# Kernel optimization log

Hardware: AMD Instinct MI355X
Metric: run time of the kernel (lower is better)

The kernel has to match this reference:

```python
import jax, jax.numpy as jnp
import numpy as np

# dims: Q queries, K hops (topk), N relation groups, M padded nodes/group
Q, K, N, M = 64, 2, 32, 64
E, D, R, S = 256, 1024, 200, 8192  # embs_size, model_size, n_rel, seq positions


def setup_inputs() -> dict:
    key = jax.random.key(0)
    ks = jax.random.split(key, 10)
    hidden_states = jax.random.normal(ks[0], (S, D), jnp.float32)
    nodes = jax.random.normal(ks[1], (Q, K, N, M, E), jnp.float32)
    # ragged groups: zero-pad beyond a random valid length (mirrors F.pad + stack)
    lengths = jax.random.randint(ks[2], (Q, K, N), 1, M + 1)
    valid = jnp.arange(M)[None, None, None, :] < lengths[..., None]
    nodes = nodes * valid[..., None]
    prob_idx = jax.random.randint(ks[3], (Q, K, N), 0, R)
    gnn_idx = jnp.arange(Q, dtype=jnp.int32)          # gnn_mask positions
    rel_idx = jnp.arange(Q, dtype=jnp.int32) + Q      # rel_mask positions (disjoint)
    sc = lambda fan: float(1.0 / np.sqrt(fan))
    u = lambda k, shp, fan: jax.random.uniform(k, shp, jnp.float32, -sc(fan), sc(fan))
    Wc = u(ks[4], (D, R), D); bc = jnp.zeros((R,), jnp.float32)
    Wq = u(ks[5], (D, D), D); bq = jnp.zeros((D,), jnp.float32)
    Wn = u(ks[6], (E, D), E); bn = jnp.zeros((D,), jnp.float32)
    Wg = u(ks[7], (E, D), E); bg = jnp.zeros((D,), jnp.float32)
    return {"hidden_states": hidden_states, "nodes": nodes, "prob_idx": prob_idx,
            "gnn_idx": gnn_idx, "rel_idx": rel_idx,
            "Wc": Wc, "bc": bc, "Wq": Wq, "bq": bq,
            "Wn": Wn, "bn": bn, "Wg": Wg, "bg": bg}


def reference(hidden_states, nodes, prob_idx, gnn_idx, rel_idx,
              Wc, bc, Wq, bq, Wn, bn, Wg, bg):
    Qn, Kn, Nn, Mn, En = nodes.shape
    # classification_head: Linear + Softmax over relations
    rel_prob = jax.nn.softmax(hidden_states[rel_idx] @ Wc + bc, axis=1)  # [Q,R]
    # gather per-group relation probabilities (extract_values_from_tensor)
    probs = jnp.take_along_axis(rel_prob, prob_idx.reshape(Qn, Kn * Nn), axis=1)
    probs = probs.reshape(Qn, Kn, Nn)                                     # [Q,K,N]
    # mask from first feature of padded node embeddings (as in calculate_scores)
    mask = nodes[..., 0] != 0                                             # [Q,K,N,M]
    # query_reprj and nodes_reprj (Linear + Tanh)
    gq = jnp.tanh(hidden_states[gnn_idx] @ Wq + bq)                       # [Q,D]
    gn = jnp.tanh(jnp.einsum('qknme,ed->qknmd', nodes, Wn) + bn)          # [Q,K,N,M,D]
    dots = jnp.einsum('qknmd,qd->qknm', gn, gq)                           # [Q,K,N,M]
    attn = jax.nn.softmax(dots, axis=3)            # softmax over nodes within group
    logits = attn * probs[..., None] / 0.1         # scale by group prob / temperature
    # global softmax over all (group, node) slots per (query, hop)
    wa = jax.nn.softmax(logits.reshape(Qn, Kn, Nn * Mn), axis=-1)
    wa = wa.reshape(Qn, Kn, Nn, Mn)
    wa = jnp.where(mask, wa, 0.0)
    # weighted mean over the flattened N*M slots, then mean over topk hops
    mean_emb = jnp.mean(nodes * wa[..., None], axis=(2, 3))               # [Q,K,E]
    pooled = mean_emb.mean(axis=1)                                        # [Q,E]
    out = jnp.tanh(pooled @ Wg + bg)                                      # gnn_reprj
    return hidden_states.at[gnn_idx].add(out)
```

## Files before the change

### kernel.cpp

```cpp
#include <hip/hip_runtime.h>
#include <hip/hip_bf16.h>
#include <math.h>

#define QDIM 64
#define KDIM 2
#define NDIM 32
#define MDIM 64
#define EDIM 256
#define DDIM 1024
#define RDIM 200
#define SDIM 8192
#define GCOUNT (QDIM * KDIM * NDIM)

typedef short short8_t __attribute__((ext_vector_type(8)));
typedef float f32x4 __attribute__((ext_vector_type(4)));

__device__ __forceinline__ float tanh_c(float x) {
    float e = __expf(2.0f * x);
    return 1.0f - 2.0f * __builtin_amdgcn_rcpf(1.0f + e);
}

__device__ __forceinline__ uint32_t f2bf(float f) {
    uint32_t u = __float_as_uint(f);
    return (u + 0x7fffu + ((u >> 16) & 1u)) >> 16;
}
__device__ __forceinline__ float bf2f(unsigned short h) {
    return __uint_as_float(((uint32_t)h) << 16);
}

__global__ __launch_bounds__(256) void prologue_kernel(
    const float* __restrict__ hs, float* __restrict__ out,
    const float* __restrict__ Wn, short* __restrict__ wnpk,
    const int* __restrict__ gnn_idx, const float* __restrict__ Wq,
    const float* __restrict__ bq, float* __restrict__ gqo,
    const int* __restrict__ rel_idx, const float* __restrict__ Wc,
    const float* __restrict__ bc, float* __restrict__ rel_prob,
    const float* __restrict__ nodes, int* __restrict__ nvarr) {
    const int b = blockIdx.x, t = threadIdx.x;
    __shared__ float row[DDIM];
    __shared__ float arr[256];

    if (b < 2048) {
        const float4* src = (const float4*)hs;
        float4* dst = (float4*)out;
        int i = b * 256 + t;
#pragma unroll
        for (int r = 0; r < 4; ++r) dst[i + r * 524288] = src[i + r * 524288];
    } else if (b < 2176) {
        int tid = (b - 2048) * 256 + t;
        int lane = tid & 63, ks = (tid >> 6) & 7, ntg = tid >> 9;
        int low = lane & 15, hi = lane >> 4;
        short8_t o;
#pragma unroll
        for (int j = 0; j < 8; ++j) {
            int k = ks * 32 + hi * 8 + j;
            int d = ntg * 16 + low;
            o[j] = (short)f2bf(Wn[(size_t)k * DDIM + d]);
        }
        *(short8_t*)(wnpk + (size_t)tid * 8) = o;
    } else if (b < 2432) {
        int bb = b - 2176;
        int q = bb >> 2, seg = bb & 3;
        const float* src = hs + (size_t)gnn_idx[q] * DDIM;
        for (int i = t; i < DDIM; i += 256) row[i] = src[i];
        __syncthreads();
        int d = seg * 256 + t;
        float a = bq[d];
#pragma unroll 8
        for (int k = 0; k < DDIM; ++k) a += row[k] * Wq[(size_t)k * DDIM + d];
        gqo[(size_t)q * DDIM + d] = tanh_c(a);
    } else if (b < 2496) {
        int q = b - 2432;
        const float* src = hs + (size_t)rel_idx[q] * DDIM;
        for (int i = t; i < DDIM; i += 256) row[i] = src[i];
        __syncthreads();
        float lg = -INFINITY;
        if (t < RDIM) {
            float a = bc[t];
            for (int k = 0; k < DDIM; ++k) a += row[k] * Wc[(size_t)k * RDIM + t];
            lg = a;
        }
        arr[t] = lg;
        __syncthreads();
        for (int s = 128; s > 0; s >>= 1) {
            if (t < s) arr[t] = fmaxf(arr[t], arr[t + s]);
            __syncthreads();
        }
        float mx = arr[0];
        __syncthreads();
        float ex = (t < RDIM) ? __expf(lg - mx) : 0.0f;
        arr[t] = ex;
        __syncthreads();
        for (int s = 128; s > 0; s >>= 1) {
            if (t < s) arr[t] += arr[t + s];
            __syncthreads();
        }
        float sm = arr[0];
        if (t < RDIM) rel_prob[q * RDIM + t] = ex / sm;
    } else {
        int g = (b - 2496) * 4 + (t >> 6);
        int lane = t & 63;
        float f0 = nodes[(size_t)g * (MDIM * EDIM) + (size_t)lane * EDIM];
        unsigned long long mk = __ballot(f0 != 0.0f);
        if (lane == 0) nvarr[g] = __popcll(mk);
    }
}

__global__ __launch_bounds__(64) void pack_jobs(const int* __restrict__ nvarr,
                                                const float* __restrict__ bn,
                                                const float* __restrict__ gq,
                                                int4* __restrict__ glist4,
                                                float* __restrict__ cqarr) {
    int q = blockIdx.x, t = threadIdx.x;
    __shared__ int lists[4][64];
    __shared__ int cnt[4];
    float cp = 0.f;
#pragma unroll
    for (int i = 0; i < 16; ++i) {
        int d = i * 64 + t;
        cp += tanh_c(bn[d]) * gq[(size_t)q * DDIM + d];
    }
#pragma unroll
    for (int off = 32; off > 0; off >>= 1) cp += __shfl_xor(cp, off);
    if (t == 0) cqarr[q] = cp;

    if (t < 4) cnt[t] = 0;
    __syncthreads();
    int g = q * 64 + t;
    int nv = nvarr[g];
    int mt = (nv + 15) >> 4;
    if (mt < 1) mt = 1;
    if (mt > 4) mt = 4;
    int pos = atomicAdd(&cnt[mt - 1], 1);
    lists[mt - 1][pos] = g;
    __syncthreads();
    if (t == 0) {
        int c1 = cnt[0], c2 = cnt[1], c3 = cnt[2], c4 = cnt[3];
        int i1 = 0, i2 = 0, i3 = 0, i4 = 0, j = 0;
        int4* outp = glist4 + q * 64;
        const int D = GCOUNT;
        while (i4 < c4) outp[j++] = make_int4(lists[3][i4++] | (0 << 20), D, D, D);
        while (i3 < c3) {
            int g1 = (i1 < c1) ? lists[0][i1++] : D;
            outp[j++] = make_int4(lists[2][i3++] | (1 << 20), g1, D, D);
        }
        while (i2 + 1 < c2) {
            int a = lists[1][i2++], b2 = lists[1][i2++];
            outp[j++] = make_int4(a | (2 << 20), b2, D, D);
        }
        if (i2 < c2) {
            int a = lists[1][i2++];
            int b2 = (i1 < c1) ? lists[0][i1++] : D;
            int c = (i1 < c1) ? lists[0][i1++] : D;
            outp[j++] = make_int4(a | (3 << 20), b2, c, D);
        }
        while (i1 < c1) {
            int a = lists[0][i1++];
            int b2 = (i1 < c1) ? lists[0][i1++] : D;
            int c = (i1 < c1) ? lists[0][i1++] : D;
            int d2 = (i1 < c1) ? lists[0][i1++] : D;
            outp[j++] = make_int4(a | (4 << 20), b2, c, d2);
        }
        while (j < 64) outp[j++] = make_int4(-1, -1, -1, -1);
    }
}

template <int U0, int NU>
__device__ __forceinline__ void epi(int g, int q, float (&dacc)[4][4],
                                    short8_t (&af)[4][8], float cq, float* scr,
                                    const float* __restrict__ rel_prob,
                                    const int* __restrict__ prob_idx,
                                    float* __restrict__ gvec, float* __restrict__ gden,
                                    float* __restrict__ gmx, int lane) {
    const int low = lane & 15, hi = lane >> 4;
    constexpr int TAIL = 64 - NU * 16;
    float mx = -INFINITY;
#pragma unroll
    for (int u = U0; u < U0 + NU; ++u)
#pragma unroll
        for (int jj = 0; jj < 4; ++jj) mx = fmaxf(mx, dacc[u][jj]);
    mx = fmaxf(mx, __shfl_xor(mx, 16));
    mx = fmaxf(mx, __shfl_xor(mx, 32));
    if (TAIL > 0) mx = fmaxf(mx, cq);
    float exv[4][4];
    float sm = 0.f;
#pragma unroll
    for (int u = U0; u < U0 + NU; ++u)
#pragma unroll
        for (int jj = 0; jj < 4; ++jj) {
            exv[u][jj] = __expf(dacc[u][jj] - mx);
            sm += exv[u][jj];
        }
    sm += __shfl_xor(sm, 16);
    sm += __shfl_xor(sm, 32);
    float ext = __expf(cq - mx);
    if (TAIL > 0) sm += (float)TAIL * ext;
    float pr = rel_prob[(size_t)q * RDIM + prob_idx[g >= GCOUNT ? 0 : g]];
    float p10 = pr * 10.0f / sm;
#pragma unroll
    for (int u = U0; u < U0 + NU; ++u)
#pragma unroll
        for (int jj = 0; jj < 4; ++jj) exv[u][jj] *= p10;
    float lgvt = ext * p10;
    float gm = -INFINITY;
#pragma unroll
    for (int u = U0; u < U0 + NU; ++u)
#pragma unroll
        for (int jj = 0; jj < 4; ++jj) gm = fmaxf(gm, exv[u][jj]);
    gm = fmaxf(gm, __shfl_xor(gm, 16));
    gm = fmaxf(gm, __shfl_xor(gm, 32));
    if (TAIL > 0) gm = fmaxf(gm, lgvt);
    float elv[4][4];
    float den = 0.f;
#pragma unroll
    for (int u = U0; u < U0 + NU; ++u)
#pragma unroll
        for (int jj = 0; jj < 4; ++jj) {
            elv[u][jj] = __expf(exv[u][jj] - gm);
            den += elv[u][jj];
        }
    den += __shfl_xor(den, 16);
    den += __shfl_xor(den, 32);
    if (TAIL > 0) den += (float)TAIL * __expf(lgvt - gm);
    if (lane == 0) {
        gden[g] = den;
        gmx[g] = gm;
    }
    float* lvarr = scr;
    float* mkarr = scr + 64;
    float* vb = scr + 128;
    if (low == 0) {
#pragma unroll
        for (int u = U0; u < U0 + NU; ++u)
#pragma unroll
            for (int jj = 0; jj < 4; ++jj) lvarr[u * 16 + hi * 4 + jj] = elv[u][jj];
    }
    asm volatile("s_waitcnt lgkmcnt(0)" ::: "memory");
    float lvm[4];
#pragma unroll
    for (int u = U0; u < U0 + NU; ++u) lvm[u] = lvarr[u * 16 + low] * mkarr[u * 16 + low];
#pragma unroll
    for (int ks = 0; ks < 8; ++ks) {
        float acj[8];
#pragma unroll
        for (int j = 0; j < 8; ++j) acj[j] = 0.f;
#pragma unroll
        for (int u = U0; u < U0 + NU; ++u) {
#pragma unroll
            for (int j = 0; j < 8; ++j)
                acj[j] += bf2f((unsigned short)af[u][ks][j]) * lvm[u];
        }
#pragma unroll
        for (int j = 0; j < 8; ++j) {
            float a = acj[j];
            a += __shfl_xor(a, 1);
            a += __shfl_xor(a, 2);
            a += __shfl_xor(a, 4);
            a += __shfl_xor(a, 8);
            if (low == 0) vb[ks * 32 + hi * 8 + j] = a;
        }
    }
    asm volatile("s_waitcnt lgkmcnt(0)" ::: "memory");
    float4 ov = ((const float4*)vb)[lane];
    *(float4*)(gvec + (size_t)g * EDIM + lane * 4) = ov;
    asm volatile("s_waitcnt lgkmcnt(0)" ::: "memory");
}

#define STEP(CUR, NXT, NTG)                                                              \
    {                                                                                    \
        int pn_ = (NTG) + 1;                                                             \
        pn_ = pn_ > 63 ? 63 : pn_;                                                       \
        const short8_t* pp_ = bbase + (size_t)pn_ * 512;                                 \
        _Pragma("unroll") for (int ks = 0; ks < 8; ++ks) NXT[ks] = pp_[ks * 64];         \
        float2 pv_ = pairs[(NTG) * 16 + low];                                            \
        f32x4 a0 = {0.f, 0.f, 0.f, 0.f}, a1 = a0, a2 = a0, a3 = a0;                      \
        _Pragma("unroll") for (int ks = 0; ks < 8; ++ks) {                               \
            a0 = __builtin_amdgcn_mfma_f32_16x16x32_bf16(af[0][ks], CUR[ks], a0, 0, 0, 0); \
            a1 = __builtin_amdgcn_mfma_f32_16x16x32_bf16(af[1][ks], CUR[ks], a1, 0, 0, 0); \
            a2 = __builtin_amdgcn_mfma_f32_16x16x32_bf16(af[2][ks], CUR[ks], a2, 0, 0, 0); \
            a3 = __builtin_amdgcn_mfma_f32_16x16x32_bf16(af[3][ks], CUR[ks], a3, 0, 0, 0); \
        }                                                                                \
        float bnv_ = pv_.x, gqv_ = pv_.y;                                                \
        _Pragma("unroll") for (int jj = 0; jj < 4; ++jj) {                               \
            dacc[0][jj] += tanh_c(a0[jj] + bnv_) * gqv_;                                 \
            dacc[1][jj] += tanh_c(a1[jj] + bnv_) * gqv_;                                 \
            dacc[2][jj] += tanh_c(a2[jj] + bnv_) * gqv_;                                 \
            dacc[3][jj] += tanh_c(a3[jj] + bnv_) * gqv_;                                 \
        }                                                                                \
    }

__global__ __launch_bounds__(64, 2) void phase1_mfma(
    const float* __restrict__ nodes, const short* __restrict__ wnpk,
    const float* __restrict__ bn, const float* __restrict__ gq,
    const float* __restrict__ rel_prob, const int* __restrict__ prob_idx,
    const int4* __restrict__ glist4, const float* __restrict__ cqarr,
    float* __restrict__ gvec, float* __restrict__ gden, float* __restrict__ gmx) {
    __shared__ alignas(16) char transit[8192];
    __shared__ float scr[384];
    int4 jb = glist4[blockIdx.x];
    if (jb.x < 0) return;
    const int shape = (jb.x >> 20) & 7;
    const int g0 = jb.x & 0xFFFF, g1 = jb.y, g2 = jb.z, g3 = jb.w;
    const int q = g0 >> 6;
    const int lane = threadIdx.x & 63;
    const int low = lane & 15, hi = lane >> 4;
    const float cqv = cqarr[q];

    const unsigned tabs[5] = {0x30201000u, 0x01201000u, 0x11011000u, 0x02011000u,
                              0x03020100u};
    const unsigned tb = tabs[shape];

    short8_t af[4][8];
#pragma unroll
    for (int u = 0; u < 4; ++u) {
        int byte_ = (tb >> (u * 8)) & 0xFF;
        int slot = byte_ & 0xF, tile = byte_ >> 4;
        int gs = slot == 0 ? g0 : slot == 1 ? g1 : slot == 2 ? g2 : g3;
        int lg = (gs >= GCOUNT) ? 0 : gs;
        const float4* src = (const float4*)(nodes + ((size_t)lg * MDIM + tile * 16) * EDIM);
#pragma unroll
        for (int i = 0; i < 16; ++i) {
            int idx4 = i * 64 + lane;
            float4 v = src[idx4];
            int r = idx4 >> 6, c4 = idx4 & 63;
            int off = (r * 512 + c4 * 8) ^ ((r & 7) << 4);
            uint32_t w0 = f2bf(v.x) | (f2bf(v.y) << 16);
            uint32_t w1 = f2bf(v.z) | (f2bf(v.w) << 16);
            *(uint2*)(transit + off) = make_uint2(w0, w1);
        }
        asm volatile("s_waitcnt lgkmcnt(0)" ::: "memory");
#pragma unroll
        for (int ks = 0; ks < 8; ++ks) {
            int off = (low * 512 + ks * 64 + hi * 16) ^ ((low & 7) << 4);
            af[u][ks] = *(const short8_t*)(transit + off);
        }
        asm volatile("s_waitcnt lgkmcnt(0)" ::: "memory");
    }

    {
        const float* gqrow = gq + (size_t)q * DDIM;
        float2* pw = (float2*)transit;
#pragma unroll
        for (int i = 0; i < 16; ++i) {
            int d = i * 64 + lane;
            float2 v;
            v.x = bn[d];
            v.y = gqrow[d];
            pw[d] = v;
        }
        asm volatile("s_waitcnt lgkmcnt(0)" ::: "memory");
    }
    const float2* pairs = (const float2*)transit;

    float dacc[4][4];
#pragma unroll
    for (int u = 0; u < 4; ++u)
#pragma unroll
        for (int jj = 0; jj < 4; ++jj) dacc[u][jj] = 0.f;
    const short8_t* bbase = (const short8_t*)wnpk + lane;
    short8_t bA[8], bB[8];
#pragma unroll
    for (int ks = 0; ks < 8; ++ks) bA[ks] = bbase[ks * 64];
    for (int it = 0; it < 32; ++it) {
        STEP(bA, bB, 2 * it);
        STEP(bB, bA, 2 * it + 1);
    }

#pragma unroll
    for (int u = 0; u < 4; ++u)
#pragma unroll
        for (int jj = 0; jj < 4; ++jj) {
            float v = dacc[u][jj];
            v += __shfl_xor(v, 1);
            v += __shfl_xor(v, 2);
            v += __shfl_xor(v, 4);
            v += __shfl_xor(v, 8);
            dacc[u][jj] = v;
        }

    if (hi == 0) {
#pragma unroll
        for (int u = 0; u < 4; ++u) {
            unsigned short s0 = (unsigned short)af[u][0][0];
            (scr + 64)[u * 16 + low] = ((s0 & 0x7fffu) != 0) ? 1.0f : 0.0f;
        }
    }
    asm volatile("s_waitcnt lgkmcnt(0)" ::: "memory");

    switch (shape) {
        case 0:
            epi<0, 4>(g0, q, dacc, af, cqv, scr, rel_prob, prob_idx, gvec, gden, gmx, lane);
            break;
        case 1:
            epi<0, 3>(g0, q, dacc, af, cqv, scr, rel_prob, prob_idx, gvec, gden, gmx, lane);
            epi<3, 1>(g1, q, dacc, af, cqv, scr, rel_prob, prob_idx, gvec, gden, gmx, lane);
            break;
        case 2:
            epi<0, 2>(g0, q, dacc, af, cqv, scr, rel_prob, prob_idx, gvec, gden, gmx, lane);
            epi<2, 2>(g1, q, dacc, af, cqv, scr, rel_prob, prob_idx, gvec, gden, gmx, lane);
            break;
        case 3:
            epi<0, 2>(g0, q, dacc, af, cqv, scr, rel_prob, prob_idx, gvec, gden, gmx, lane);
            epi<2, 1>(g1, q, dacc, af, cqv, scr, rel_prob, prob_idx, gvec, gden, gmx, lane);
            epi<3, 1>(g2, q, dacc, af, cqv, scr, rel_prob, prob_idx, gvec, gden, gmx, lane);
            break;
        default:
            epi<0, 1>(g0, q, dacc, af, cqv, scr, rel_prob, prob_idx, gvec, gden, gmx, lane);
            epi<1, 1>(g1, q, dacc, af, cqv, scr, rel_prob, prob_idx, gvec, gden, gmx, lane);
            epi<2, 1>(g2, q, dacc, af, cqv, scr, rel_prob, prob_idx, gvec, gden, gmx, lane);
            epi<3, 1>(g3, q, dacc, af, cqv, scr, rel_prob, prob_idx, gvec, gden, gmx, lane);
            break;
    }
}

__global__ __launch_bounds__(256) void combine_kernel(const float* __restrict__ gvec,
                                                      const float* __restrict__ gden,
                                                      const float* __restrict__ gmx,
                                                      float* __restrict__ memb) {
    int qk = blockIdx.x, t = threadIdx.x;
    __shared__ float sgm[NDIM], sden[NDIM];
    if (t < NDIM) {
        sgm[t] = gmx[qk * NDIM + t];
        sden[t] = gden[qk * NDIM + t];
    }
    __syncthreads();
    float gm = -INFINITY;
    for (int n = 0; n < NDIM; ++n) gm = fmaxf(gm, sgm[n]);
    float gs = 0.f;
    for (int n = 0; n < NDIM; ++n) gs += sden[n] * __expf(sgm[n] - gm);
    float me = 0.f;
    for (int n = 0; n < NDIM; ++n)
        me += gvec[(size_t)(qk * NDIM + n) * EDIM + t] * __expf(sgm[n] - gm);
    memb[(size_t)qk * EDIM + t] = me / (gs * (float)(NDIM * MDIM));
}

__global__ __launch_bounds__(256) void out_kernel(const float* __restrict__ memb,
                                                  const float* __restrict__ Wg,
                                                  const float* __restrict__ bg,
                                                  const int* __restrict__ gnn_idx,
                                                  float* __restrict__ out) {
    int q = blockIdx.x, t = threadIdx.x;
    __shared__ float pooled[EDIM];
    pooled[t] = 0.5f * (memb[(size_t)(q * 2 + 0) * EDIM + t] + memb[(size_t)(q * 2 + 1) * EDIM + t]);
    __syncthreads();
    float4 a = ((const float4*)bg)[t];
    const float4* Wg4 = (const float4*)Wg;
    for (int e = 0; e < EDIM; ++e) {
        float p = pooled[e];
        float4 w = Wg4[(size_t)e * (DDIM / 4) + t];
        a.x += p * w.x; a.y += p * w.y; a.z += p * w.z; a.w += p * w.w;
    }
    float4* op = (float4*)(out + (size_t)gnn_idx[q] * DDIM);
    float4 cur = op[t];
    cur.x += tanh_c(a.x);
    cur.y += tanh_c(a.y);
    cur.z += tanh_c(a.z);
    cur.w += tanh_c(a.w);
    op[t] = cur;
}

extern "C" void kernel_launch(void* const* d_in, const int* in_sizes, int n_in,
                              void* d_out, int out_size, void* d_ws, size_t ws_size,
                              hipStream_t stream) {
    const float* hs = (const float*)d_in[0];
    const float* nodes = (const float*)d_in[1];
    const int* prob_idx = (const int*)d_in[2];
    const int* gnn_idx = (const int*)d_in[3];
    const int* rel_idx = (const int*)d_in[4];
    const float* Wc = (const float*)d_in[5];
    const float* bc = (const float*)d_in[6];
    const float* Wq = (const float*)d_in[7];
    const float* bq = (const float*)d_in[8];
    const float* Wn = (const float*)d_in[9];
    const float* bn = (const float*)d_in[10];
    const float* Wg = (const float*)d_in[11];
    const float* bg = (const float*)d_in[12];
    float* out = (float*)d_out;
    float* ws = (float*)d_ws;

    float* relprob = ws;
    float* gqbuf = ws + 16384;
    float* gvec = gqbuf + 65536;
    float* gdenA = gvec + 1048832;
    float* gmaxA = gdenA + 4352;
    float* membuf = gmaxA + 4352;
    short* wnpk = (short*)(membuf + 32768);
    int* nvarr = (int*)(ws + 1303296);
    int4* glist4 = (int4*)(ws + 1307392);
    float* cqarr = ws + 1323776;

    prologue_kernel<<<3520, 256, 0, stream>>>(hs, out, Wn, wnpk, gnn_idx, Wq, bq,
                                              gqbuf, rel_idx, Wc, bc, relprob,
                                              nodes, nvarr);
    pack_jobs<<<QDIM, 64, 0, stream>>>(nvarr, bn, gqbuf, glist4, cqarr);
    phase1_mfma<<<GCOUNT, 64, 0, stream>>>(nodes, wnpk, bn, gqbuf, relprob,
                                           prob_idx, glist4, cqarr, gvec, gdenA, gmaxA);
    combine_kernel<<<QDIM * KDIM, 256, 0, stream>>>(gvec, gdenA, gmaxA, membuf);
    out_kernel<<<QDIM, 256, 0, stream>>>(membuf, Wg, bg, gnn_idx, out);
}
```

Before: 301.0 us.

## Split each MFMA job across two waves and pack two jobs per block

The phase1 kernel moves from one 64-thread wave per job, each holding four 16-row node tiles, to 256-thread blocks that process two jobs. Each wave now holds two tiles, which halves the per-wave A-fragment registers and MFMA chain length and exposes more parallel waves. The group softmax epilogue and weighted-sum reduction are rebuilt to go through shared memory with block barriers, and bias/query pairs are loaded once per block. In exchange, each wave re-reads the full Wn stream for only two tiles, so total Wn traffic per job doubles. The change also adds barriers and LDS usage that may limit occupancy.

```diff
diff --git a/kernel.cpp b/kernel.cpp
--- a/kernel.cpp
+++ b/kernel.cpp
@@ -165,251 +165,234 @@
     }
 }
 
-template <int U0, int NU>
-__device__ __forceinline__ void epi(int g, int q, float (&dacc)[4][4],
-                                    short8_t (&af)[4][8], float cq, float* scr,
-                                    const float* __restrict__ rel_prob,
-                                    const int* __restrict__ prob_idx,
-                                    float* __restrict__ gvec, float* __restrict__ gden,
-                                    float* __restrict__ gmx, int lane) {
-    const int low = lane & 15, hi = lane >> 4;
-    constexpr int TAIL = 64 - NU * 16;
-    float mx = -INFINITY;
-#pragma unroll
-    for (int u = U0; u < U0 + NU; ++u)
-#pragma unroll
-        for (int jj = 0; jj < 4; ++jj) mx = fmaxf(mx, dacc[u][jj]);
-    mx = fmaxf(mx, __shfl_xor(mx, 16));
-    mx = fmaxf(mx, __shfl_xor(mx, 32));
-    if (TAIL > 0) mx = fmaxf(mx, cq);
-    float exv[4][4];
-    float sm = 0.f;
-#pragma unroll
-    for (int u = U0; u < U0 + NU; ++u)
-#pragma unroll
-        for (int jj = 0; jj < 4; ++jj) {
-            exv[u][jj] = __expf(dacc[u][jj] - mx);
-            sm += exv[u][jj];
-        }
-    sm += __shfl_xor(sm, 16);
-    sm += __shfl_xor(sm, 32);
-    float ext = __expf(cq - mx);
-    if (TAIL > 0) sm += (float)TAIL * ext;
-    float pr = rel_prob[(size_t)q * RDIM + prob_idx[g >= GCOUNT ? 0 : g]];
-    float p10 = pr * 10.0f / sm;
-#pragma unroll
-    for (int u = U0; u < U0 + NU; ++u)
-#pragma unroll
-        for (int jj = 0; jj < 4; ++jj) exv[u][jj] *= p10;
-    float lgvt = ext * p10;
-    float gm = -INFINITY;
-#pragma unroll
-    for (int u = U0; u < U0 + NU; ++u)
-#pragma unroll
-        for (int jj = 0; jj < 4; ++jj) gm = fmaxf(gm, exv[u][jj]);
-    gm = fmaxf(gm, __shfl_xor(gm, 16));
-    gm = fmaxf(gm, __shfl_xor(gm, 32));
-    if (TAIL > 0) gm = fmaxf(gm, lgvt);
-    float elv[4][4];
-    float den = 0.f;
-#pragma unroll
-    for (int u = U0; u < U0 + NU; ++u)
-#pragma unroll
-        for (int jj = 0; jj < 4; ++jj) {
-            elv[u][jj] = __expf(exv[u][jj] - gm);
-            den += elv[u][jj];
-        }
-    den += __shfl_xor(den, 16);
-    den += __shfl_xor(den, 32);
-    if (TAIL > 0) den += (float)TAIL * __expf(lgvt - gm);
-    if (lane == 0) {
-        gden[g] = den;
-        gmx[g] = gm;
-    }
-    float* lvarr = scr;
-    float* mkarr = scr + 64;
-    float* vb = scr + 128;
-    if (low == 0) {
-#pragma unroll
-        for (int u = U0; u < U0 + NU; ++u)
-#pragma unroll
-            for (int jj = 0; jj < 4; ++jj) lvarr[u * 16 + hi * 4 + jj] = elv[u][jj];
-    }
-    asm volatile("s_waitcnt lgkmcnt(0)" ::: "memory");
-    float lvm[4];
-#pragma unroll
-    for (int u = U0; u < U0 + NU; ++u) lvm[u] = lvarr[u * 16 + low] * mkarr[u * 16 + low];
-#pragma unroll
-    for (int ks = 0; ks < 8; ++ks) {
-        float acj[8];
-#pragma unroll
-        for (int j = 0; j < 8; ++j) acj[j] = 0.f;
-#pragma unroll
-        for (int u = U0; u < U0 + NU; ++u) {
-#pragma unroll
-            for (int j = 0; j < 8; ++j)
-                acj[j] += bf2f((unsigned short)af[u][ks][j]) * lvm[u];
-        }
-#pragma unroll
-        for (int j = 0; j < 8; ++j) {
-            float a = acj[j];
-            a += __shfl_xor(a, 1);
-            a += __shfl_xor(a, 2);
-            a += __shfl_xor(a, 4);
-            a += __shfl_xor(a, 8);
-            if (low == 0) vb[ks * 32 + hi * 8 + j] = a;
-        }
-    }
-    asm volatile("s_waitcnt lgkmcnt(0)" ::: "memory");
-    float4 ov = ((const float4*)vb)[lane];
-    *(float4*)(gvec + (size_t)g * EDIM + lane * 4) = ov;
-    asm volatile("s_waitcnt lgkmcnt(0)" ::: "memory");
-}
-
-#define STEP(CUR, NXT, NTG)                                                              \
-    {                                                                                    \
-        int pn_ = (NTG) + 1;                                                             \
-        pn_ = pn_ > 63 ? 63 : pn_;                                                       \
-        const short8_t* pp_ = bbase + (size_t)pn_ * 512;                                 \
-        _Pragma("unroll") for (int ks = 0; ks < 8; ++ks) NXT[ks] = pp_[ks * 64];         \
-        float2 pv_ = pairs[(NTG) * 16 + low];                                            \
-        f32x4 a0 = {0.f, 0.f, 0.f, 0.f}, a1 = a0, a2 = a0, a3 = a0;                      \
-        _Pragma("unroll") for (int ks = 0; ks < 8; ++ks) {                               \
+#define STEP2(CUR, NXT, NTG)                                                               \
+    {                                                                                      \
+        int pn_ = (NTG) + 1;                                                               \
+        pn_ = pn_ > 63 ? 63 : pn_;                                                         \
+        const short8_t* pp_ = bbase + (size_t)pn_ * 512;                                   \
+        _Pragma("unroll") for (int ks = 0; ks < 8; ++ks) NXT[ks] = pp_[ks * 64];           \
+        float2 pv_ = pairs[(NTG)*16 + low];                                                \
+        f32x4 a0 = {0.f, 0.f, 0.f, 0.f}, a1 = a0;                                          \
+        _Pragma("unroll") for (int ks = 0; ks < 8; ++ks) {                                 \
             a0 = __builtin_amdgcn_mfma_f32_16x16x32_bf16(af[0][ks], CUR[ks], a0, 0, 0, 0); \
             a1 = __builtin_amdgcn_mfma_f32_16x16x32_bf16(af[1][ks], CUR[ks], a1, 0, 0, 0); \
-            a2 = __builtin_amdgcn_mfma_f32_16x16x32_bf16(af[2][ks], CUR[ks], a2, 0, 0, 0); \
-            a3 = __builtin_amdgcn_mfma_f32_16x16x32_bf16(af[3][ks], CUR[ks], a3, 0, 0, 0); \
-        }                                                                                \
-        float bnv_ = pv_.x, gqv_ = pv_.y;                                                \
-        _Pragma("unroll") for (int jj = 0; jj < 4; ++jj) {                               \
-            dacc[0][jj] += tanh_c(a0[jj] + bnv_) * gqv_;                                 \
-            dacc[1][jj] += tanh_c(a1[jj] + bnv_) * gqv_;                                 \
-            dacc[2][jj] += tanh_c(a2[jj] + bnv_) * gqv_;                                 \
-            dacc[3][jj] += tanh_c(a3[jj] + bnv_) * gqv_;                                 \
-        }                                                                                \
-    }
-
-__global__ __launch_bounds__(64, 2) void phase1_mfma(
+        }                                                                                  \
+        float bnv_ = pv_.x, gqv_ = pv_.y;                                                  \
+        _Pragma("unroll") for (int jj = 0; jj < 4; ++jj) {                                 \
+            dacc[0][jj] += tanh_c(a0[jj] + bnv_) * gqv_;                                   \
+            dacc[1][jj] += tanh_c(a1[jj] + bnv_) * gqv_;                                   \
+        }                                                                                  \
+    }
+
+__global__ __launch_bounds__(256, 3) void phase1_mfma(
     const float* __restrict__ nodes, const short* __restrict__ wnpk,
     const float* __restrict__ bn, const float* __restrict__ gq,
     const float* __restrict__ rel_prob, const int* __restrict__ prob_idx,
     const int4* __restrict__ glist4, const float* __restrict__ cqarr,
     float* __restrict__ gvec, float* __restrict__ gden, float* __restrict__ gmx) {
-    __shared__ alignas(16) char transit[8192];
-    __shared__ float scr[384];
-    int4 jb = glist4[blockIdx.x];
-    if (jb.x < 0) return;
-    const int shape = (jb.x >> 20) & 7;
-    const int g0 = jb.x & 0xFFFF, g1 = jb.y, g2 = jb.z, g3 = jb.w;
-    const int q = g0 >> 6;
-    const int lane = threadIdx.x & 63;
+    __shared__ alignas(16) char transit[4][8192];
+    __shared__ float2 pairs[DDIM];
+    __shared__ float vecu[8][EDIM];
+    __shared__ float dots_s[128];
+    __shared__ float lv_s[128];
+    __shared__ float mk_s[128];
+
+    const int tid = threadIdx.x;
+    const int w = tid >> 6, lane = tid & 63;
     const int low = lane & 15, hi = lane >> 4;
+
+    const int4 jb0 = glist4[2 * blockIdx.x];
+    const int4 jb1 = glist4[2 * blockIdx.x + 1];
+    if (jb0.x < 0 && jb1.x < 0) return;
+    const int4 jb = (w < 2) ? jb0 : jb1;
+    const bool live = jb.x >= 0;
+    const int q = ((jb0.x >= 0 ? jb0.x : jb1.x) & 0xFFFF) >> 6;
     const float cqv = cqarr[q];
 
     const unsigned tabs[5] = {0x30201000u, 0x01201000u, 0x11011000u, 0x02011000u,
                               0x03020100u};
-    const unsigned tb = tabs[shape];
-
-    short8_t af[4][8];
-#pragma unroll
-    for (int u = 0; u < 4; ++u) {
-        int byte_ = (tb >> (u * 8)) & 0xFF;
-        int slot = byte_ & 0xF, tile = byte_ >> 4;
-        int gs = slot == 0 ? g0 : slot == 1 ? g1 : slot == 2 ? g2 : g3;
-        int lg = (gs >= GCOUNT) ? 0 : gs;
-        const float4* src = (const float4*)(nodes + ((size_t)lg * MDIM + tile * 16) * EDIM);
-#pragma unroll
-        for (int i = 0; i < 16; ++i) {
-            int idx4 = i * 64 + lane;
-            float4 v = src[idx4];
-            int r = idx4 >> 6, c4 = idx4 & 63;
-            int off = (r * 512 + c4 * 8) ^ ((r & 7) << 4);
-            uint32_t w0 = f2bf(v.x) | (f2bf(v.y) << 16);
-            uint32_t w1 = f2bf(v.z) | (f2bf(v.w) << 16);
-            *(uint2*)(transit + off) = make_uint2(w0, w1);
-        }
-        asm volatile("s_waitcnt lgkmcnt(0)" ::: "memory");
-#pragma unroll
-        for (int ks = 0; ks < 8; ++ks) {
-            int off = (low * 512 + ks * 64 + hi * 16) ^ ((low & 7) << 4);
-            af[u][ks] = *(const short8_t*)(transit + off);
-        }
-        asm volatile("s_waitcnt lgkmcnt(0)" ::: "memory");
+    const int gA[4] = {jb.x & 0xFFFF, jb.y, jb.z, jb.w};
+    const unsigned tb = live ? tabs[(jb.x >> 20) & 7] : 0;
+
+    int usrc[2] = {GCOUNT, GCOUNT};
+    short8_t af[2][8];
+    if (live) {
+        char* ldsw = transit[w];
+#pragma unroll
+        for (int u2 = 0; u2 < 2; ++u2) {
+            int u = (w & 1) * 2 + u2;
+            int byte_ = (tb >> (u * 8)) & 0xFF;
+            int slot = byte_ & 0xF, tile = byte_ >> 4;
+            int gs = gA[slot];
+            usrc[u2] = gs;
+            int lg = (gs >= GCOUNT) ? 0 : gs;
+            const float4* src =
+                (const float4*)(nodes + ((size_t)lg * MDIM + tile * 16) * EDIM);
+#pragma unroll
+            for (int i = 0; i < 16; ++i) {
+                int idx4 = i * 64 + lane;
+                float4 v = src[idx4];
+                int r = idx4 >> 6, c4 = idx4 & 63;
+                int off = (r * 512 + c4 * 8) ^ ((r & 7) << 4);
+                uint32_t w0 = f2bf(v.x) | (f2bf(v.y) << 16);
+                uint32_t w1 = f2bf(v.z) | (f2bf(v.w) << 16);
+                *(uint2*)(ldsw + off) = make_uint2(w0, w1);
+            }
+            asm volatile("s_waitcnt lgkmcnt(0)" ::: "memory");
+#pragma unroll
+            for (int ks = 0; ks < 8; ++ks) {
+                int off = (low * 512 + ks * 64 + hi * 16) ^ ((low & 7) << 4);
+                af[u2][ks] = *(const short8_t*)(ldsw + off);
+            }
+            asm volatile("s_waitcnt lgkmcnt(0)" ::: "memory");
+        }
     }
 
     {
         const float* gqrow = gq + (size_t)q * DDIM;
-        float2* pw = (float2*)transit;
-#pragma unroll
-        for (int i = 0; i < 16; ++i) {
-            int d = i * 64 + lane;
-            float2 v;
-            v.x = bn[d];
-            v.y = gqrow[d];
-            pw[d] = v;
-        }
-        asm volatile("s_waitcnt lgkmcnt(0)" ::: "memory");
-    }
-    const float2* pairs = (const float2*)transit;
-
-    float dacc[4][4];
-#pragma unroll
-    for (int u = 0; u < 4; ++u)
-#pragma unroll
-        for (int jj = 0; jj < 4; ++jj) dacc[u][jj] = 0.f;
-    const short8_t* bbase = (const short8_t*)wnpk + lane;
-    short8_t bA[8], bB[8];
-#pragma unroll
-    for (int ks = 0; ks < 8; ++ks) bA[ks] = bbase[ks * 64];
-    for (int it = 0; it < 32; ++it) {
-        STEP(bA, bB, 2 * it);
-        STEP(bB, bA, 2 * it + 1);
-    }
-
-#pragma unroll
-    for (int u = 0; u < 4; ++u)
-#pragma unroll
-        for (int jj = 0; jj < 4; ++jj) {
-            float v = dacc[u][jj];
-            v += __shfl_xor(v, 1);
-            v += __shfl_xor(v, 2);
-            v += __shfl_xor(v, 4);
-            v += __shfl_xor(v, 8);
-            dacc[u][jj] = v;
-        }
-
-    if (hi == 0) {
-#pragma unroll
-        for (int u = 0; u < 4; ++u) {
-            unsigned short s0 = (unsigned short)af[u][0][0];
-            (scr + 64)[u * 16 + low] = ((s0 & 0x7fffu) != 0) ? 1.0f : 0.0f;
-        }
-    }
-    asm volatile("s_waitcnt lgkmcnt(0)" ::: "memory");
-
-    switch (shape) {
-        case 0:
-            epi<0, 4>(g0, q, dacc, af, cqv, scr, rel_prob, prob_idx, gvec, gden, gmx, lane);
-            break;
-        case 1:
-            epi<0, 3>(g0, q, dacc, af, cqv, scr, rel_prob, prob_idx, gvec, gden, gmx, lane);
-            epi<3, 1>(g1, q, dacc, af, cqv, scr, rel_prob, prob_idx, gvec, gden, gmx, lane);
-            break;
-        case 2:
-            epi<0, 2>(g0, q, dacc, af, cqv, scr, rel_prob, prob_idx, gvec, gden, gmx, lane);
-            epi<2, 2>(g1, q, dacc, af, cqv, scr, rel_prob, prob_idx, gvec, gden, gmx, lane);
-            break;
-        case 3:
-            epi<0, 2>(g0, q, dacc, af, cqv, scr, rel_prob, prob_idx, gvec, gden, gmx, lane);
-            epi<2, 1>(g1, q, dacc, af, cqv, scr, rel_prob, prob_idx, gvec, gden, gmx, lane);
-            epi<3, 1>(g2, q, dacc, af, cqv, scr, rel_prob, prob_idx, gvec, gden, gmx, lane);
-            break;
-        default:
-            epi<0, 1>(g0, q, dacc, af, cqv, scr, rel_prob, prob_idx, gvec, gden, gmx, lane);
-            epi<1, 1>(g1, q, dacc, af, cqv, scr, rel_prob, prob_idx, gvec, gden, gmx, lane);
-            epi<2, 1>(g2, q, dacc, af, cqv, scr, rel_prob, prob_idx, gvec, gden, gmx, lane);
-            epi<3, 1>(g3, q, dacc, af, cqv, scr, rel_prob, prob_idx, gvec, gden, gmx, lane);
-            break;
+#pragma unroll
+        for (int i = 0; i < 4; ++i) {
+            int d = tid + i * 256;
+            pairs[d] = make_float2(bn[d], gqrow[d]);
+        }
+    }
+    __syncthreads();
+
+    float dacc[2][4] = {};
+    if (live) {
+        const short8_t* bbase = (const short8_t*)wnpk + lane;
+        short8_t bA[8], bB[8];
+#pragma unroll
+        for (int ks = 0; ks < 8; ++ks) bA[ks] = bbase[ks * 64];
+        for (int it = 0; it < 32; ++it) {
+            STEP2(bA, bB, 2 * it);
+            STEP2(bB, bA, 2 * it + 1);
+        }
+#pragma unroll
+        for (int u2 = 0; u2 < 2; ++u2)
+#pragma unroll
+            for (int jj = 0; jj < 4; ++jj) {
+                float v = dacc[u2][jj];
+                v += __shfl_xor(v, 1);
+                v += __shfl_xor(v, 2);
+                v += __shfl_xor(v, 4);
+                v += __shfl_xor(v, 8);
+                dacc[u2][jj] = v;
+            }
+        if (low == 0) {
+#pragma unroll
+            for (int u2 = 0; u2 < 2; ++u2)
+#pragma unroll
+                for (int jj = 0; jj < 4; ++jj)
+                    dots_s[(w * 2 + u2) * 16 + hi * 4 + jj] = dacc[u2][jj];
+        }
+        if (hi == 0) {
+#pragma unroll
+            for (int u2 = 0; u2 < 2; ++u2) {
+                unsigned short s0 = (unsigned short)af[u2][0][0];
+                mk_s[(w * 2 + u2) * 16 + low] = ((s0 & 0x7fffu) != 0) ? 1.0f : 0.0f;
+            }
+        }
+    }
+    __syncthreads();
+
+    const int NGT[5] = {1, 2, 2, 3, 4};
+    const int U0T[5][4] = {{0, 0, 0, 0}, {0, 3, 0, 0}, {0, 2, 0, 0},
+                           {0, 2, 3, 0}, {0, 1, 2, 3}};
+    const int NUT[5][4] = {{4, 0, 0, 0}, {3, 1, 0, 0}, {2, 2, 0, 0},
+                           {2, 1, 1, 0}, {1, 1, 1, 1}};
+    const int ng0 = (jb0.x >= 0) ? NGT[(jb0.x >> 20) & 7] : 0;
+    const int ng1 = (jb1.x >= 0) ? NGT[(jb1.x >> 20) & 7] : 0;
+    const int ngtot = ng0 + ng1;
+
+    for (int gi = w; gi < ngtot; gi += 4) {
+        int jx = (gi < ng0) ? 0 : 1;
+        int4 J = jx ? jb1 : jb0;
+        int li = jx ? gi - ng0 : gi;
+        int shp = (J.x >> 20) & 7;
+        int U0 = U0T[shp][li] + jx * 4;
+        int NU = NUT[shp][li];
+        int gg = (li == 0) ? (J.x & 0xFFFF) : (li == 1) ? J.y : (li == 2) ? J.z : J.w;
+        if (gg >= GCOUNT) continue;
+        int NS = NU * 16, TL = 64 - NS;
+        float dv = (lane < NS) ? dots_s[U0 * 16 + lane] : -INFINITY;
+        float mx = dv;
+#pragma unroll
+        for (int o = 32; o > 0; o >>= 1) mx = fmaxf(mx, __shfl_xor(mx, o));
+        if (TL > 0) mx = fmaxf(mx, cqv);
+        float ex = (lane < NS) ? __expf(dv - mx) : 0.f;
+        float sm = ex;
+#pragma unroll
+        for (int o = 32; o > 0; o >>= 1) sm += __shfl_xor(sm, o);
+        float ext = __expf(cqv - mx);
+        if (TL > 0) sm += (float)TL * ext;
+        float pr = rel_prob[(size_t)q * RDIM + prob_idx[gg]];
+        float p10 = pr * 10.0f / sm;
+        float l2 = ex * p10;
+        float lgvt = ext * p10;
+        float gm = (lane < NS) ? l2 : -INFINITY;
+#pragma unroll
+        for (int o = 32; o > 0; o >>= 1) gm = fmaxf(gm, __shfl_xor(gm, o));
+        if (TL > 0) gm = fmaxf(gm, lgvt);
+        float el = (lane < NS) ? __expf(l2 - gm) : 0.f;
+        float den = el;
+#pragma unroll
+        for (int o = 32; o > 0; o >>= 1) den += __shfl_xor(den, o);
+        if (TL > 0) den += (float)TL * __expf(lgvt - gm);
+        if (lane < NS) lv_s[U0 * 16 + lane] = el * mk_s[U0 * 16 + lane];
+        if (lane == 0) {
+            gden[gg] = den;
+            gmx[gg] = gm;
+        }
+    }
+    __syncthreads();
+
+    if (live) {
+#pragma unroll
+        for (int u2 = 0; u2 < 2; ++u2) {
+            if (usrc[u2] >= GCOUNT) continue;
+            int ug = w * 2 + u2;
+            float lvm = lv_s[ug * 16 + low];
+#pragma unroll
+            for (int ks = 0; ks < 8; ++ks) {
+                float acj[8];
+#pragma unroll
+                for (int j = 0; j < 8; ++j)
+                    acj[j] = bf2f((unsigned short)af[u2][ks][j]) * lvm;
+#pragma unroll
+                for (int j = 0; j < 8; ++j) {
+                    float a = acj[j];
+                    a += __shfl_xor(a, 1);
+                    a += __shfl_xor(a, 2);
+                    a += __shfl_xor(a, 4);
+                    a += __shfl_xor(a, 8);
+                    acj[j] = a;
+                }
+                if (low == 0) {
+#pragma unroll
+                    for (int j = 0; j < 8; ++j) vecu[ug][ks * 32 + hi * 8 + j] = acj[j];
+                }
+            }
+        }
+    }
+    __syncthreads();
+
+    for (int gi = w; gi < ngtot; gi += 4) {
+        int jx = (gi < ng0) ? 0 : 1;
+        int4 J = jx ? jb1 : jb0;
+        int li = jx ? gi - ng0 : gi;
+        int shp = (J.x >> 20) & 7;
+        int U0 = U0T[shp][li] + jx * 4;
+        int NU = NUT[shp][li];
+        int gg = (li == 0) ? (J.x & 0xFFFF) : (li == 1) ? J.y : (li == 2) ? J.z : J.w;
+        if (gg >= GCOUNT) continue;
+#pragma unroll 4
+        for (int c = 0; c < 4; ++c) {
+            int e = c * 64 + lane;
+            float s = 0.f;
+            for (int uu = 0; uu < NU; ++uu) s += vecu[U0 + uu][e];
+            gvec[(size_t)gg * EDIM + e] = s;
+        }
     }
 }
 
@@ -493,8 +476,9 @@
                                               gqbuf, rel_idx, Wc, bc, relprob,
                                               nodes, nvarr);
     pack_jobs<<<QDIM, 64, 0, stream>>>(nvarr, bn, gqbuf, glist4, cqarr);
-    phase1_mfma<<<GCOUNT, 64, 0, stream>>>(nodes, wnpk, bn, gqbuf, relprob,
-                                           prob_idx, glist4, cqarr, gvec, gdenA, gmaxA);
+    phase1_mfma<<<GCOUNT / 2, 256, 0, stream>>>(nodes, wnpk, bn, gqbuf, relprob,
+                                                prob_idx, glist4, cqarr, gvec, gdenA,
+                                                gmaxA);
     combine_kernel<<<QDIM * KDIM, 256, 0, stream>>>(gvec, gdenA, gmaxA, membuf);
     out_kernel<<<QDIM, 256, 0, stream>>>(membuf, Wg, bg, gnn_idx, out);
 }
```

Measured after the change: 263.9 us. 12.3% less time.

## Pack four wave jobs per block, load node fragments directly, fuse combine and output

Applied to the files above, without the earlier changes.

The phase1 kernel now runs four 64-lane waves per 256-thread block. The waves share one bias/query pair table in LDS, loaded once per block, instead of each wave filling its own. Node A-fragments are read straight from global memory and converted to bf16 in registers, which drops the LDS transit staging and its waits. The combine and output kernels are merged into one launch per query, removing an intermediate buffer and a launch. Risks are less coalesced strided global reads for the fragments, a different job-to-block mapping that depends on pack_jobs layout, and an extra block barrier.

```diff
diff --git a/kernel.cpp b/kernel.cpp
--- a/kernel.cpp
+++ b/kernel.cpp
@@ -195,7 +195,7 @@
     sm += __shfl_xor(sm, 32);
     float ext = __expf(cq - mx);
     if (TAIL > 0) sm += (float)TAIL * ext;
-    float pr = rel_prob[(size_t)q * RDIM + prob_idx[g >= GCOUNT ? 0 : g]];
+    float pr = rel_prob[(size_t)q * RDIM + prob_idx[g]];
     float p10 = pr * 10.0f / sm;
 #pragma unroll
     for (int u = U0; u < U0 + NU; ++u)
@@ -272,7 +272,7 @@
         pn_ = pn_ > 63 ? 63 : pn_;                                                       \
         const short8_t* pp_ = bbase + (size_t)pn_ * 512;                                 \
         _Pragma("unroll") for (int ks = 0; ks < 8; ++ks) NXT[ks] = pp_[ks * 64];         \
-        float2 pv_ = pairs[(NTG) * 16 + low];                                            \
+        float2 pv_ = pairs[(NTG)*16 + low];                                              \
         f32x4 a0 = {0.f, 0.f, 0.f, 0.f}, a1 = a0, a2 = a0, a3 = a0;                      \
         _Pragma("unroll") for (int ks = 0; ks < 8; ++ks) {                               \
             a0 = __builtin_amdgcn_mfma_f32_16x16x32_bf16(af[0][ks], CUR[ks], a0, 0, 0, 0); \
@@ -289,22 +289,36 @@
         }                                                                                \
     }
 
-__global__ __launch_bounds__(64, 2) void phase1_mfma(
+__global__ __launch_bounds__(256, 2) void phase1_mfma(
     const float* __restrict__ nodes, const short* __restrict__ wnpk,
     const float* __restrict__ bn, const float* __restrict__ gq,
     const float* __restrict__ rel_prob, const int* __restrict__ prob_idx,
     const int4* __restrict__ glist4, const float* __restrict__ cqarr,
     float* __restrict__ gvec, float* __restrict__ gden, float* __restrict__ gmx) {
-    __shared__ alignas(16) char transit[8192];
-    __shared__ float scr[384];
-    int4 jb = glist4[blockIdx.x];
-    if (jb.x < 0) return;
-    const int shape = (jb.x >> 20) & 7;
-    const int g0 = jb.x & 0xFFFF, g1 = jb.y, g2 = jb.z, g3 = jb.w;
-    const int q = g0 >> 6;
-    const int lane = threadIdx.x & 63;
+    __shared__ float2 pairs[DDIM];
+    __shared__ float scr4[4][384];
+    const int tid = threadIdx.x;
+    const int w = tid >> 6, lane = tid & 63;
     const int low = lane & 15, hi = lane >> 4;
+
+    if (glist4[blockIdx.x * 4].x < 0) return;
+    const int q = blockIdx.x >> 4;
     const float cqv = cqarr[q];
+    const int4 jb = glist4[blockIdx.x * 4 + w];
+    const bool live = jb.x >= 0;
+    const int shape = live ? ((jb.x >> 20) & 7) : 0;
+    const int gA[4] = {jb.x & 0xFFFF, jb.y, jb.z, jb.w};
+
+    {
+        const float* gqrow = gq + (size_t)q * DDIM;
+#pragma unroll
+        for (int i = 0; i < 4; ++i) {
+            int d = tid + i * 256;
+            pairs[d] = make_float2(bn[d], gqrow[d]);
+        }
+    }
+    __syncthreads();
+    if (!live) return;
 
     const unsigned tabs[5] = {0x30201000u, 0x01201000u, 0x11011000u, 0x02011000u,
                               0x03020100u};
@@ -315,42 +329,31 @@
     for (int u = 0; u < 4; ++u) {
         int byte_ = (tb >> (u * 8)) & 0xFF;
         int slot = byte_ & 0xF, tile = byte_ >> 4;
-        int gs = slot == 0 ? g0 : slot == 1 ? g1 : slot == 2 ? g2 : g3;
+        int gs = gA[slot];
         int lg = (gs >= GCOUNT) ? 0 : gs;
-        const float4* src = (const float4*)(nodes + ((size_t)lg * MDIM + tile * 16) * EDIM);
-#pragma unroll
-        for (int i = 0; i < 16; ++i) {
-            int idx4 = i * 64 + lane;
-            float4 v = src[idx4];
-            int r = idx4 >> 6, c4 = idx4 & 63;
-            int off = (r * 512 + c4 * 8) ^ ((r & 7) << 4);
-            uint32_t w0 = f2bf(v.x) | (f2bf(v.y) << 16);
-            uint32_t w1 = f2bf(v.z) | (f2bf(v.w) << 16);
-            *(uint2*)(transit + off) = make_uint2(w0, w1);
-        }
-        asm volatile("s_waitcnt lgkmcnt(0)" ::: "memory");
+        const float* rowp =
+            nodes + ((size_t)lg * MDIM + tile * 16 + low) * EDIM + hi * 8;
 #pragma unroll
         for (int ks = 0; ks < 8; ++ks) {
-            int off = (low * 512 + ks * 64 + hi * 16) ^ ((low & 7) << 4);
-            af[u][ks] = *(const short8_t*)(transit + off);
-        }
-        asm volatile("s_waitcnt lgkmcnt(0)" ::: "memory");
-    }
-
-    {
-        const float* gqrow = gq + (size_t)q * DDIM;
-        float2* pw = (float2*)transit;
-#pragma unroll
-        for (int i = 0; i < 16; ++i) {
-            int d = i * 64 + lane;
-            float2 v;
-            v.x = bn[d];
-            v.y = gqrow[d];
-            pw[d] = v;
-        }
-        asm volatile("s_waitcnt lgkmcnt(0)" ::: "memory");
-    }
-    const float2* pairs = (const float2*)transit;
+            float4 a = *(const float4*)(rowp + ks * 32);
+            float4 b = *(const float4*)(rowp + ks * 32 + 4);
+            short8_t o;
+            o[0] = (short)f2bf(a.x); o[1] = (short)f2bf(a.y);
+            o[2] = (short)f2bf(a.z); o[3] = (short)f2bf(a.w);
+            o[4] = (short)f2bf(b.x); o[5] = (short)f2bf(b.y);
+            o[6] = (short)f2bf(b.z); o[7] = (short)f2bf(b.w);
+            af[u][ks] = o;
+        }
+    }
+
+    float* scr = scr4[w];
+    if (hi == 0) {
+#pragma unroll
+        for (int u = 0; u < 4; ++u) {
+            unsigned short s0 = (unsigned short)af[u][0][0];
+            (scr + 64)[u * 16 + low] = ((s0 & 0x7fffu) != 0) ? 1.0f : 0.0f;
+        }
+    }
 
     float dacc[4][4];
 #pragma unroll
@@ -378,70 +381,63 @@
             dacc[u][jj] = v;
         }
 
-    if (hi == 0) {
-#pragma unroll
-        for (int u = 0; u < 4; ++u) {
-            unsigned short s0 = (unsigned short)af[u][0][0];
-            (scr + 64)[u * 16 + low] = ((s0 & 0x7fffu) != 0) ? 1.0f : 0.0f;
-        }
-    }
-    asm volatile("s_waitcnt lgkmcnt(0)" ::: "memory");
-
     switch (shape) {
         case 0:
-            epi<0, 4>(g0, q, dacc, af, cqv, scr, rel_prob, prob_idx, gvec, gden, gmx, lane);
+            epi<0, 4>(gA[0], q, dacc, af, cqv, scr, rel_prob, prob_idx, gvec, gden, gmx, lane);
             break;
         case 1:
-            epi<0, 3>(g0, q, dacc, af, cqv, scr, rel_prob, prob_idx, gvec, gden, gmx, lane);
-            epi<3, 1>(g1, q, dacc, af, cqv, scr, rel_prob, prob_idx, gvec, gden, gmx, lane);
+            epi<0, 3>(gA[0], q, dacc, af, cqv, scr, rel_prob, prob_idx, gvec, gden, gmx, lane);
+            epi<3, 1>(gA[1], q, dacc, af, cqv, scr, rel_prob, prob_idx, gvec, gden, gmx, lane);
             break;
         case 2:
-            epi<0, 2>(g0, q, dacc, af, cqv, scr, rel_prob, prob_idx, gvec, gden, gmx, lane);
-            epi<2, 2>(g1, q, dacc, af, cqv, scr, rel_prob, prob_idx, gvec, gden, gmx, lane);
+            epi<0, 2>(gA[0], q, dacc, af, cqv, scr, rel_prob, prob_idx, gvec, gden, gmx, lane);
+            epi<2, 2>(gA[1], q, dacc, af, cqv, scr, rel_prob, prob_idx, gvec, gden, gmx, lane);
             break;
         case 3:
-            epi<0, 2>(g0, q, dacc, af, cqv, scr, rel_prob, prob_idx, gvec, gden, gmx, lane);
-            epi<2, 1>(g1, q, dacc, af, cqv, scr, rel_prob, prob_idx, gvec, gden, gmx, lane);
-            epi<3, 1>(g2, q, dacc, af, cqv, scr, rel_prob, prob_idx, gvec, gden, gmx, lane);
+            epi<0, 2>(gA[0], q, dacc, af, cqv, scr, rel_prob, prob_idx, gvec, gden, gmx, lane);
+            epi<2, 1>(gA[1], q, dacc, af, cqv, scr, rel_prob, prob_idx, gvec, gden, gmx, lane);
+            epi<3, 1>(gA[2], q, dacc, af, cqv, scr, rel_prob, prob_idx, gvec, gden, gmx, lane);
             break;
         default:
-            epi<0, 1>(g0, q, dacc, af, cqv, scr, rel_prob, prob_idx, gvec, gden, gmx, lane);
-            epi<1, 1>(g1, q, dacc, af, cqv, scr, rel_prob, prob_idx, gvec, gden, gmx, lane);
-            epi<2, 1>(g2, q, dacc, af, cqv, scr, rel_prob, prob_idx, gvec, gden, gmx, lane);
-            epi<3, 1>(g3, q, dacc, af, cqv, scr, rel_prob, prob_idx, gvec, gden, gmx, lane);
+            epi<0, 1>(gA[0], q, dacc, af, cqv, scr, rel_prob, prob_idx, gvec, gden, gmx, lane);
+            if (gA[1] < GCOUNT)
+                epi<1, 1>(gA[1], q, dacc, af, cqv, scr, rel_prob, prob_idx, gvec, gden, gmx, lane);
+            if (gA[2] < GCOUNT)
+                epi<2, 1>(gA[2], q, dacc, af, cqv, scr, rel_prob, prob_idx, gvec, gden, gmx, lane);
+            if (gA[3] < GCOUNT)
+                epi<3, 1>(gA[3], q, dacc, af, cqv, scr, rel_prob, prob_idx, gvec, gden, gmx, lane);
             break;
     }
 }
 
-__global__ __launch_bounds__(256) void combine_kernel(const float* __restrict__ gvec,
-                                                      const float* __restrict__ gden,
-                                                      const float* __restrict__ gmx,
-                                                      float* __restrict__ memb) {
-    int qk = blockIdx.x, t = threadIdx.x;
-    __shared__ float sgm[NDIM], sden[NDIM];
-    if (t < NDIM) {
-        sgm[t] = gmx[qk * NDIM + t];
-        sden[t] = gden[qk * NDIM + t];
+__global__ __launch_bounds__(256) void combineout_kernel(
+    const float* __restrict__ gvec, const float* __restrict__ gden,
+    const float* __restrict__ gmx, const float* __restrict__ Wg,
+    const float* __restrict__ bg, const int* __restrict__ gnn_idx,
+    float* __restrict__ out) {
+    int q = blockIdx.x, t = threadIdx.x;
+    __shared__ float sgm[2][NDIM], sden[2][NDIM];
+    __shared__ float pooled[EDIM];
+    if (t < 64) {
+        int k = t >> 5, n = t & 31;
+        sgm[k][n] = gmx[(q * 2 + k) * NDIM + n];
+        sden[k][n] = gden[(q * 2 + k) * NDIM + n];
     }
     __syncthreads();
-    float gm = -INFINITY;
-    for (int n = 0; n < NDIM; ++n) gm = fmaxf(gm, sgm[n]);
-    float gs = 0.f;
-    for (int n = 0; n < NDIM; ++n) gs += sden[n] * __expf(sgm[n] - gm);
-    float me = 0.f;
-    for (int n = 0; n < NDIM; ++n)
-        me += gvec[(size_t)(qk * NDIM + n) * EDIM + t] * __expf(sgm[n] - gm);
-    memb[(size_t)qk * EDIM + t] = me / (gs * (float)(NDIM * MDIM));
-}
-
-__global__ __launch_bounds__(256) void out_kernel(const float* __restrict__ memb,
-                                                  const float* __restrict__ Wg,
-                                                  const float* __restrict__ bg,
-                                                  const int* __restrict__ gnn_idx,
-                                                  float* __restrict__ out) {
-    int q = blockIdx.x, t = threadIdx.x;
-    __shared__ float pooled[EDIM];
-    pooled[t] = 0.5f * (memb[(size_t)(q * 2 + 0) * EDIM + t] + memb[(size_t)(q * 2 + 1) * EDIM + t]);
+    float pl = 0.f;
+#pragma unroll
+    for (int k = 0; k < 2; ++k) {
+        float gm = -INFINITY;
+        for (int n = 0; n < NDIM; ++n) gm = fmaxf(gm, sgm[k][n]);
+        float gs = 0.f;
+        for (int n = 0; n < NDIM; ++n) gs += sden[k][n] * __expf(sgm[k][n] - gm);
+        float me = 0.f;
+        for (int n = 0; n < NDIM; ++n)
+            me += gvec[(size_t)((q * 2 + k) * NDIM + n) * EDIM + t] *
+                  __expf(sgm[k][n] - gm);
+        pl += 0.5f * me / (gs * (float)(NDIM * MDIM));
+    }
+    pooled[t] = pl;
     __syncthreads();
     float4 a = ((const float4*)bg)[t];
     const float4* Wg4 = (const float4*)Wg;
@@ -493,8 +489,9 @@
                                               gqbuf, rel_idx, Wc, bc, relprob,
                                               nodes, nvarr);
     pack_jobs<<<QDIM, 64, 0, stream>>>(nvarr, bn, gqbuf, glist4, cqarr);
-    phase1_mfma<<<GCOUNT, 64, 0, stream>>>(nodes, wnpk, bn, gqbuf, relprob,
-                                           prob_idx, glist4, cqarr, gvec, gdenA, gmaxA);
-    combine_kernel<<<QDIM * KDIM, 256, 0, stream>>>(gvec, gdenA, gmaxA, membuf);
-    out_kernel<<<QDIM, 256, 0, stream>>>(membuf, Wg, bg, gnn_idx, out);
-}
+    phase1_mfma<<<QDIM * 16, 256, 0, stream>>>(nodes, wnpk, bn, gqbuf, relprob,
+                                               prob_idx, glist4, cqarr, gvec, gdenA,
+                                               gmaxA);
+    combineout_kernel<<<QDIM, 256, 0, stream>>>(gvec, gdenA, gmaxA, Wg, bg, gnn_idx,
+                                                out);
+}
```

After: 391.5 us. 1.3x slower.
